# Performance work log

Measured on AMD Instinct MI355X. Metric: run time of the kernel, lower is better.

Reference implementation:

```python
import jax, jax.numpy as jnp
import numpy as np
from jax import lax

VOCAB = 50000; EMB = 256; HID = 256; NLAYERS = 2; OUT = 4
MAXLEN = 32; BATCH = 512; BEAM = 4


def lstm_step(h, c, x, Wih, Whh, bih, bhh):
    # h, c: [L, B, H]; x: [B, E]; torch gate order i, f, g, o
    hs, cs = [], []
    inp = x
    for l in range(Wih.shape[0]):
        g = inp @ Wih[l].T + h[l] @ Whh[l].T + bih[l] + bhh[l]
        i, f, gg, o = jnp.split(g, 4, axis=-1)
        cn = jax.nn.sigmoid(f) * c[l] + jax.nn.sigmoid(i) * jnp.tanh(gg)
        hn = jax.nn.sigmoid(o) * jnp.tanh(cn)
        hs.append(hn); cs.append(cn); inp = hn
    return jnp.stack(hs), jnp.stack(cs), inp


def encode(tokens, emb, Wih, Whh, bih, bhh):
    # tokens: [T, B] int
    x = emb[tokens]  # [T, B, E]
    L, H = Whh.shape[0], Whh.shape[2]
    h0 = jnp.zeros((L, tokens.shape[1], H), x.dtype)

    def step(carry, xt):
        h, c = carry
        h, c, _ = lstm_step(h, c, xt, Wih, Whh, bih, bhh)
        return (h, c), None

    (h, c), _ = lax.scan(step, (h0, h0), x)
    return h, c


def decode_step(tok, h, c, emb, Wih, Whh, bih, bhh, fcW, fcb):
    x = emb[tok]
    h, c, top = lstm_step(h, c, x, Wih, Whh, bih, bhh)
    out = jax.nn.log_softmax(top @ fcW.T + fcb, axis=-1)  # [B', V]
    return out, h, c


def _forward(src, enc_emb, enc_Wih, enc_Whh, enc_bih, enc_bhh,
             dec_emb, dec_Wih, dec_Whh, dec_bih, dec_bhh, dec_fcW, dec_fcb,
             beam_width, teacher_force):
    T, B = src.shape[1], src.shape[2]
    V = dec_fcb.shape[0]
    K = beam_width
    # torch.flip(src[:, 1:, :], [1]): reverse time axis
    h, c = encode(src[0, 1:, :][::-1], enc_emb, enc_Wih, enc_Whh, enc_bih, enc_bhh)

    dec = lambda tok, h, c: decode_step(tok, h, c, dec_emb, dec_Wih, dec_Whh,
                                        dec_bih, dec_bhh, dec_fcW, dec_fcb)

    if teacher_force:
        def step(carry, tok):
            h, c = carry
            out, h, c = dec(tok, h, c)
            return (h, c), out
        _, outs = lax.scan(step, (h, c), src[0])
        return outs

    # --- batch beam search; flat row layout is beam-major: row k*B + b ---
    h = jnp.tile(h, (1, K, 1)); c = jnp.tile(c, (1, K, 1))
    out0, h, c = dec(jnp.tile(src[0, 0, :], K), h, c)  # [B*K, V]
    outputs = jnp.zeros((T, B * K, V), out0.dtype).at[0].set(out0)
    # backtrack[0] = argmax token -> cumulative path score starts at row max
    cum = jnp.max(out0, axis=1)  # [B*K]
    batch_ix = jnp.tile(jnp.arange(B), K)

    def step(carry, xs):
        h, c, cum, outputs = carry
        tok_t, t = xs
        out, h, c = dec(jnp.tile(tok_t, K), h, c)  # [B*K, V]
        probs = cum[:, None] + out  # unnormalized path scores
        # chunk over beams, concat along columns -> [B, K*V]
        probs_b = probs.reshape(K, B, V).transpose(1, 0, 2).reshape(B, K * V)
        lp = (5.0 + t) / 6.0  # length penalty, LP_ALPHA = 1
        _, top_idx = lax.top_k(probs_b / lp, K)  # [B, K]
        rows = (top_idx // V).T.reshape(-1) * B + batch_ix  # [B*K] source rows
        tks = (top_idx % V).T.reshape(-1)  # chosen tokens per new beam row
        h = h[:, rows, :]; c = c[:, rows, :]
        outputs = outputs[:, rows, :].at[t].set(out[rows])
        cum = cum[rows] + out[rows, tks]
        return (h, c, cum, outputs), None

    ts = jnp.arange(1, T)
    (h, c, cum, outputs), _ = lax.scan(step, (h, c, cum, outputs), (src[0, 1:, :], ts))
    return outputs[:, :B, :]


def setup_inputs() -> dict:
    key = jax.random.key(0)
    ks = jax.random.split(key, 16)
    w = lambda k, shape: jax.random.normal(k, shape, jnp.float32) * 0.1
    return {
        'src': jax.random.randint(ks[0], (1, MAXLEN, BATCH), 0, VOCAB),
        'trg': jax.random.randint(ks[1], (MAXLEN, BATCH), 0, OUT),
        'enc_emb': w(ks[2], (VOCAB, EMB)),
        'enc_Wih': w(ks[3], (NLAYERS, 4 * HID, EMB)),
        'enc_Whh': w(ks[4], (NLAYERS, 4 * HID, HID)),
        'enc_bih': w(ks[5], (NLAYERS, 4 * HID)),
        'enc_bhh': w(ks[6], (NLAYERS, 4 * HID)),
        'dec_emb': w(ks[7], (VOCAB, EMB)),
        'dec_Wih': w(ks[8], (NLAYERS, 4 * HID, EMB)),
        'dec_Whh': w(ks[9], (NLAYERS, 4 * HID, HID)),
        'dec_bih': w(ks[10], (NLAYERS, 4 * HID)),
        'dec_bhh': w(ks[11], (NLAYERS, 4 * HID)),
        'dec_fcW': w(ks[12], (OUT, HID)),
        'dec_fcb': w(ks[13], (OUT,)),
        'beam_width': BEAM,
        'teacher_force': 0,
    }


def reference(src, trg, enc_emb, enc_Wih, enc_Whh, enc_bih, enc_bhh,
              dec_emb, dec_Wih, dec_Whh, dec_bih, dec_bhh, dec_fcW, dec_fcb,
              beam_width, teacher_force):
    return _forward(src, enc_emb, enc_Wih, enc_Whh, enc_bih, enc_bhh,
                    dec_emb, dec_Wih, dec_Whh, dec_bih, dec_bhh, dec_fcW, dec_fcb,
                    beam_width, teacher_force)
```

## Files before the change

### kernel.cpp

```cpp
#include <hip/hip_runtime.h>

typedef unsigned short u16;
typedef unsigned int   u32;
typedef __attribute__((ext_vector_type(8))) short bf16x8;
typedef __attribute__((ext_vector_type(4))) float f32x4;

#define DEVINL static __device__ __forceinline__
#define MFMA __builtin_amdgcn_mfma_f32_16x16x32_bf16

DEVINL u16 f2bf(float f){ u32 x = __float_as_uint(f); return (u16)((x + 0x7fffu + ((x>>16)&1u)) >> 16); }
DEVINL float bf2f(u16 u){ return __uint_as_float(((u32)u) << 16); }
DEVINL u32 pack2(float a, float b){ return (u32)f2bf(a) | ((u32)f2bf(b) << 16); }
DEVINL float sigm(float x){ return 1.f/(1.f + __expf(-x)); }
DEVINL float tanhs(float x){ float xc = fminf(fmaxf(x,-15.f),15.f); float e = __expf(2.f*xc); return (e-1.f)/(e+1.f); }
DEVINL void g_store(u32* p, u32 v){ __hip_atomic_store(p, v, __ATOMIC_RELAXED, __HIP_MEMORY_SCOPE_AGENT); }
DEVINL u32  g_load(const u32* p){ return __hip_atomic_load(p, __ATOMIC_RELAXED, __HIP_MEMORY_SCOPE_AGENT); }

__global__ void pack_all(const float* __restrict__ eih, const float* __restrict__ ehh,
                         const float* __restrict__ dih, const float* __restrict__ dhh,
                         const float* __restrict__ ebi, const float* __restrict__ ebh,
                         const float* __restrict__ dbi, const float* __restrict__ dbh,
                         u16* __restrict__ wout, float* __restrict__ bout,
                         u32* __restrict__ flags){
  int blk = blockIdx.x, t = threadIdx.x;
  if (blk < 8192){
    int m = blk >> 10, j2 = blk & 1023;
    const float* base = (m < 4) ? ((m & 1) ? ehh : eih) : ((m & 1) ? dhh : dih);
    const float* S = base + (size_t)((m >> 1) & 1) * 262144;
    int u = j2 >> 2, g = j2 & 3, j = g*256 + u;
    wout[(size_t)blk*256 + t] = f2bf(S[(size_t)j*256 + t]);
  } else if (blk < 8208){
    int idx = (blk - 8192)*256 + t;
    int phase = idx >> 11, l = (idx >> 10) & 1, j2 = idx & 1023;
    int u = j2 >> 2, g = j2 & 3, j = g*256 + u;
    const float* bi = phase ? dbi : ebi;
    const float* bh = phase ? dbh : ebh;
    bout[idx] = bi[l*1024 + j] + bh[l*1024 + j];
  } else {
    for (int i = t; i < 2048; i += 256) flags[i] = 0u;
  }
}

struct SM {
  u16   X[16][264];
  u16   H1t[16][264];
  u16   H2t[16][264];
  float fcw[4][256];
  float fcb[4];
  int   tok[63][16];
};

__global__ void __launch_bounds__(512, 2)
lstm_main(const int* __restrict__ src, const float* __restrict__ enc_emb,
          const float* __restrict__ dec_emb, const u16* __restrict__ wpack,
          const float* __restrict__ bpack, const float* __restrict__ fcW,
          const float* __restrict__ fcb, float* __restrict__ out,
          u32* __restrict__ H1, u32* __restrict__ H2, u32* __restrict__ flags)
{
  __shared__ SM sm;
  const int tid  = threadIdx.x;
  const int wv   = tid >> 6;
  const int lane = tid & 63;
  const int agrp = lane >> 4;
  const int n    = lane & 15;
  const int gid  = blockIdx.x & 31;
  const int w    = blockIdx.x >> 5;
  const int wgb0 = gid << 4;
  const int xr   = tid >> 5, xk = (tid & 31) << 3;
  const int myl  = wv >> 2;
  const int wq   = wv & 3;
  const bool pub = (agrp & 1) == 0;
  const int jrow0 = (w << 7) + (wq << 5) + n;
  const int jrow1 = jrow0 + 16;
  const int uu0   = (w << 5) + (wq << 3) + agrp;
  const int uu1   = uu0 + 4;
  const int pw0   = (w << 4) + (wq << 2) + (agrp >> 1);
  const int pw1   = pw0 + 2;

  for (int i = tid; i < 1008; i += 512){
    int s = i >> 4, b = i & 15;
    int t = (s < 31) ? (31 - s) : (s - 31);
    sm.tok[s][b] = src[t*512 + wgb0 + b];
  }
  for (int i = tid; i < 1024; i += 512) ((float*)sm.fcw)[i] = fcW[i];
  if (tid < 4) sm.fcb[tid] = fcb[tid];
  for (int i = tid; i < 2112; i += 512){
    ((u32*)sm.H1t)[i] = 0u;
    ((u32*)sm.H2t)[i] = 0u;
  }
  __syncthreads();
  {
    int tk = sm.tok[0][xr];
    const float* e = enc_emb + (size_t)tk*256 + xk;
    float4 v0 = *(const float4*)e, v1 = *(const float4*)(e + 4);
    u32* d = (u32*)&sm.X[xr][xk];
    d[0]=pack2(v0.x,v0.y); d[1]=pack2(v0.z,v0.w); d[2]=pack2(v1.x,v1.y); d[3]=pack2(v1.z,v1.w);
  }
  float4 xh0, xh1;
  {
    int tk = sm.tok[1][xr];
    const float* e = enc_emb + (size_t)tk*256 + xk;
    xh0 = *(const float4*)e; xh1 = *(const float4*)(e + 4);
  }

  bf16x8 W[2][16];
  float4 br[2];
  float  cst[2] = {0.f, 0.f};

  auto LOADW = [&](int ph){
    const u16* base = wpack + (size_t)ph*1048576 + (size_t)myl*524288;
    #pragma unroll
    for (int kk = 0; kk < 16; kk++){
      const size_t moff = (size_t)(kk >> 3)*262144 + ((kk & 7) << 5) + (agrp << 3);
      W[0][kk] = *(const bf16x8*)(base + moff + (size_t)jrow0*256);
      W[1][kk] = *(const bf16x8*)(base + moff + (size_t)jrow1*256);
    }
    br[0] = *(const float4*)(bpack + (((ph << 1) + myl) << 10) + (uu0 << 2));
    br[1] = *(const float4*)(bpack + (((ph << 1) + myl) << 10) + (uu1 << 2));
  };
  LOADW(0);
  __syncthreads();

  auto step = [&](int t){
    const bool active = myl ? (t >= 1) : (t <= 62);
    if (active){
      const u16 (*loT)[264] = myl ? sm.H1t : sm.X;
      const u16 (*hiT)[264] = myl ? sm.H2t : sm.H1t;
      f32x4 a0 = {0.f,0.f,0.f,0.f}, a1 = {0.f,0.f,0.f,0.f};
      #pragma unroll
      for (int kk = 0; kk < 8; kk++){
        bf16x8 b = *(const bf16x8*)&loT[n][(kk << 5) + (agrp << 3)];
        a0 = MFMA(W[0][kk], b, a0, 0, 0, 0);
        a1 = MFMA(W[1][kk], b, a1, 0, 0, 0);
      }
      #pragma unroll
      for (int kk = 0; kk < 8; kk++){
        bf16x8 b = *(const bf16x8*)&hiT[n][(kk << 5) + (agrp << 3)];
        a0 = MFMA(W[0][8 + kk], b, a0, 0, 0, 0);
        a1 = MFMA(W[1][8 + kk], b, a1, 0, 0, 0);
      }
      float I0 = sigm(a0[0] + br[0].x), F0 = sigm(a0[1] + br[0].y);
      float G0 = tanhs(a0[2] + br[0].z), O0 = sigm(a0[3] + br[0].w);
      float cn0 = F0*cst[0] + I0*G0; cst[0] = cn0;
      u16 h0 = f2bf(O0 * tanhs(cn0));
      float I1 = sigm(a1[0] + br[1].x), F1 = sigm(a1[1] + br[1].y);
      float G1 = tanhs(a1[2] + br[1].z), O1 = sigm(a1[3] + br[1].w);
      float cn1 = F1*cst[1] + I1*G1; cst[1] = cn1;
      u16 h1b = f2bf(O1 * tanhs(cn1));
      u32 o0 = (u32)__shfl_xor((int)(u32)h0, 16);
      u32 o1 = (u32)__shfl_xor((int)(u32)h1b, 16);
      const int ppar = myl ? ((t + 1) & 1) : (t & 1);
      u32* Hp = (myl ? H2 : H1) + ((size_t)ppar*32 + gid)*2048 + n*128;
      if (pub){
        g_store(Hp + pw0, (u32)h0 | (o0 << 16));
        g_store(Hp + pw1, (u32)h1b | (o1 << 16));
      }
    }
    __syncthreads();
    if (tid == 0) g_store(&flags[gid*8 + w], (u32)(t + 1));
    if (wv == 0){
      const u32 tgt = (u32)(t + 1);
      const bool mine = lane < 8;
      for (;;){
        u32 v = mine ? g_load(&flags[gid*8 + lane]) : tgt;
        if (__all(v >= tgt)) break;
        __builtin_amdgcn_s_sleep(1);
      }
    } else if (wv == 1 && t >= 33){
      const int b = (w << 1) + (lane >> 5), v = (lane >> 3) & 3, q8 = lane & 7;
      const u16* hrow = &sm.H2t[b][q8 << 5];
      const float* wr = &sm.fcw[v][q8 << 5];
      float s = 0.f;
      #pragma unroll
      for (int f = 0; f < 4; f++){
        bf16x8 hv = *(const bf16x8*)(hrow + (f << 3));
        const float4 wa = *(const float4*)(wr + (f << 3));
        const float4 wb = *(const float4*)(wr + (f << 3) + 4);
        s += bf2f((u16)hv[0])*wa.x + bf2f((u16)hv[1])*wa.y
           + bf2f((u16)hv[2])*wa.z + bf2f((u16)hv[3])*wa.w
           + bf2f((u16)hv[4])*wb.x + bf2f((u16)hv[5])*wb.y
           + bf2f((u16)hv[6])*wb.z + bf2f((u16)hv[7])*wb.w;
      }
      s += __shfl_xor(s, 1); s += __shfl_xor(s, 2); s += __shfl_xor(s, 4);
      s += sm.fcb[v];
      float m = fmaxf(s, __shfl_xor(s, 8)); m = fmaxf(m, __shfl_xor(m, 16));
      float e_ = __expf(s - m);
      float es = e_ + __shfl_xor(e_, 8); es += __shfl_xor(es, 16);
      if (q8 == 0)
        out[((size_t)(t - 33)*512 + wgb0 + b)*4 + v] = s - m - __logf(es);
    }
    __syncthreads();
    {
      const int q = tid << 2, r = tid >> 5, p = q & 127;
      if (t < 63){
        const u32* h1r = H1 + ((size_t)(t & 1)*32 + gid)*2048;
        u32 v0 = g_load(h1r+q), v1 = g_load(h1r+q+1), v2 = g_load(h1r+q+2), v3 = g_load(h1r+q+3);
        u32* d1 = (u32*)&sm.H1t[r][p << 1];
        d1[0]=v0; d1[1]=v1; d1[2]=v2; d1[3]=v3;
      }
      if (t > 0){
        const u32* h2r = H2 + ((size_t)((t - 1) & 1)*32 + gid)*2048;
        u32 w0 = g_load(h2r+q), w1 = g_load(h2r+q+1), w2 = g_load(h2r+q+2), w3 = g_load(h2r+q+3);
        u32* d2 = (u32*)&sm.H2t[r][p << 1];
        d2[0]=w0; d2[1]=w1; d2[2]=w2; d2[3]=w3;
      }
      if (t + 1 < 63){
        u32* d = (u32*)&sm.X[xr][xk];
        d[0]=pack2(xh0.x,xh0.y); d[1]=pack2(xh0.z,xh0.w);
        d[2]=pack2(xh1.x,xh1.y); d[3]=pack2(xh1.z,xh1.w);
      }
      if (t + 2 < 63){
        int tk = sm.tok[t+2][xr];
        const float* e = ((t+2) < 31 ? enc_emb : dec_emb) + (size_t)tk*256 + xk;
        xh0 = *(const float4*)e; xh1 = *(const float4*)(e + 4);
      }
    }
    __syncthreads();
  };

  for (int t = 0; t <= 30; ++t) step(t);
  if (myl == 0) LOADW(1);
  step(31);
  if (myl == 1) LOADW(1);
  for (int t = 32; t <= 63; ++t) step(t);

  if (wv == 1){
    const int b = (w << 1) + (lane >> 5), v = (lane >> 3) & 3, q8 = lane & 7;
    const u16* hrow = &sm.H2t[b][q8 << 5];
    const float* wr = &sm.fcw[v][q8 << 5];
    float s = 0.f;
    #pragma unroll
    for (int f = 0; f < 4; f++){
      bf16x8 hv = *(const bf16x8*)(hrow + (f << 3));
      const float4 wa = *(const float4*)(wr + (f << 3));
      const float4 wb = *(const float4*)(wr + (f << 3) + 4);
      s += bf2f((u16)hv[0])*wa.x + bf2f((u16)hv[1])*wa.y
         + bf2f((u16)hv[2])*wa.z + bf2f((u16)hv[3])*wa.w
         + bf2f((u16)hv[4])*wb.x + bf2f((u16)hv[5])*wb.y
         + bf2f((u16)hv[6])*wb.z + bf2f((u16)hv[7])*wb.w;
    }
    s += __shfl_xor(s, 1); s += __shfl_xor(s, 2); s += __shfl_xor(s, 4);
    s += sm.fcb[v];
    float m = fmaxf(s, __shfl_xor(s, 8)); m = fmaxf(m, __shfl_xor(m, 16));
    float e_ = __expf(s - m);
    float es = e_ + __shfl_xor(e_, 8); es += __shfl_xor(es, 16);
    if (q8 == 0)
      out[((size_t)31*512 + wgb0 + b)*4 + v] = s - m - __logf(es);
  }
}

extern "C" void kernel_launch(void* const* d_in, const int* in_sizes, int n_in,
                              void* d_out, int out_size, void* d_ws, size_t ws_size,
                              hipStream_t stream){
  const int*   src     = (const int*)  d_in[0];
  const float* enc_emb = (const float*)d_in[2];
  const float* enc_Wih = (const float*)d_in[3];
  const float* enc_Whh = (const float*)d_in[4];
  const float* enc_bih = (const float*)d_in[5];
  const float* enc_bhh = (const float*)d_in[6];
  const float* dec_emb = (const float*)d_in[7];
  const float* dec_Wih = (const float*)d_in[8];
  const float* dec_Whh = (const float*)d_in[9];
  const float* dec_bih = (const float*)d_in[10];
  const float* dec_bhh = (const float*)d_in[11];
  const float* fcW     = (const float*)d_in[12];
  const float* fcb     = (const float*)d_in[13];
  float* out = (float*)d_out;
  (void)in_sizes; (void)n_in; (void)out_size; (void)ws_size;

  u16*   wpack = (u16*)d_ws;
  float* bpack = (float*)((char*)d_ws + 4194304);
  u32*   H1    = (u32*)((char*)d_ws + 4194304 + 16384);
  u32*   H2    = (u32*)((char*)d_ws + 4194304 + 16384 + 524288);
  u32*   flags = (u32*)((char*)d_ws + 4194304 + 16384 + 1048576);

  pack_all<<<8209, 256, 0, stream>>>(enc_Wih, enc_Whh, dec_Wih, dec_Whh,
                                     enc_bih, enc_bhh, dec_bih, dec_bhh,
                                     wpack, bpack, flags);
  lstm_main<<<256, 512, 0, stream>>>(src, enc_emb, dec_emb, wpack, bpack,
                                     fcW, fcb, out, H1, H2, flags);
}
```

Baseline: 246.6 us.

## Precompute input projection off critical path and split per-layer cross-block sync

Layer-0 waves now compute the input-to-hidden MFMA product for the next timestep after publishing h, so only the recurrent half stays on the critical path. The embedding staging buffer is double-buffered and prefetched one step further ahead to make this possible. Cross-workgroup flag signalling is split into separate flags for layer 1 and layer 2. Each layer's flag is raised by whichever wave finishes last, tracked with a shared-memory atomic counter, and a different wave per layer polls it. The goal is to cut per-step latency of the serial recurrence, at the cost of more LDS, more registers and more complex synchronisation.

```diff
diff --git a/kernel.cpp b/kernel.cpp
--- a/kernel.cpp
+++ b/kernel.cpp
@@ -42,12 +42,13 @@
 }
 
 struct SM {
-  u16   X[16][264];
+  u16   X[2][16][264];
   u16   H1t[16][264];
   u16   H2t[16][264];
   float fcw[4][256];
   float fcb[4];
   int   tok[63][16];
+  u32   C1, C2;
 };
 
 __global__ void __launch_bounds__(512, 2)
@@ -84,24 +85,28 @@
   }
   for (int i = tid; i < 1024; i += 512) ((float*)sm.fcw)[i] = fcW[i];
   if (tid < 4) sm.fcb[tid] = fcb[tid];
+  if (tid == 4){ sm.C1 = 0u; sm.C2 = 0u; }
   for (int i = tid; i < 2112; i += 512){
     ((u32*)sm.H1t)[i] = 0u;
     ((u32*)sm.H2t)[i] = 0u;
   }
   __syncthreads();
   {
-    int tk = sm.tok[0][xr];
+    int tk0 = sm.tok[0][xr];
+    const float* e0 = enc_emb + (size_t)tk0*256 + xk;
+    float4 a0 = *(const float4*)e0, a1 = *(const float4*)(e0 + 4);
+    u32* d0 = (u32*)&sm.X[0][xr][xk];
+    d0[0]=pack2(a0.x,a0.y); d0[1]=pack2(a0.z,a0.w); d0[2]=pack2(a1.x,a1.y); d0[3]=pack2(a1.z,a1.w);
+    int tk1 = sm.tok[1][xr];
+    const float* e1 = enc_emb + (size_t)tk1*256 + xk;
+    float4 b0 = *(const float4*)e1, b1 = *(const float4*)(e1 + 4);
+    u32* d1 = (u32*)&sm.X[1][xr][xk];
+    d1[0]=pack2(b0.x,b0.y); d1[1]=pack2(b0.z,b0.w); d1[2]=pack2(b1.x,b1.y); d1[3]=pack2(b1.z,b1.w);
+  }
+  float4 xh0, xh1;
+  { int tk = sm.tok[2][xr];
     const float* e = enc_emb + (size_t)tk*256 + xk;
-    float4 v0 = *(const float4*)e, v1 = *(const float4*)(e + 4);
-    u32* d = (u32*)&sm.X[xr][xk];
-    d[0]=pack2(v0.x,v0.y); d[1]=pack2(v0.z,v0.w); d[2]=pack2(v1.x,v1.y); d[3]=pack2(v1.z,v1.w);
-  }
-  float4 xh0, xh1;
-  {
-    int tk = sm.tok[1][xr];
-    const float* e = enc_emb + (size_t)tk*256 + xk;
-    xh0 = *(const float4*)e; xh1 = *(const float4*)(e + 4);
-  }
+    xh0 = *(const float4*)e; xh1 = *(const float4*)(e + 4); }
 
   bf16x8 W[2][16];
   float4 br[2];
@@ -121,110 +126,173 @@
   LOADW(0);
   __syncthreads();
 
+  f32x4 gxa = {0.f,0.f,0.f,0.f}, gxb = {0.f,0.f,0.f,0.f};
+  if (myl == 0){
+    #pragma unroll
+    for (int kk = 0; kk < 8; kk++){
+      bf16x8 f = *(const bf16x8*)&sm.X[0][n][(kk << 5) + (agrp << 3)];
+      gxa = MFMA(W[0][kk], f, gxa, 0, 0, 0);
+      gxb = MFMA(W[1][kk], f, gxb, 0, 0, 0);
+    }
+  }
+
   auto step = [&](int t){
-    const bool active = myl ? (t >= 1) : (t <= 62);
-    if (active){
-      const u16 (*loT)[264] = myl ? sm.H1t : sm.X;
-      const u16 (*hiT)[264] = myl ? sm.H2t : sm.H1t;
-      f32x4 a0 = {0.f,0.f,0.f,0.f}, a1 = {0.f,0.f,0.f,0.f};
-      #pragma unroll
-      for (int kk = 0; kk < 8; kk++){
-        bf16x8 b = *(const bf16x8*)&loT[n][(kk << 5) + (agrp << 3)];
-        a0 = MFMA(W[0][kk], b, a0, 0, 0, 0);
-        a1 = MFMA(W[1][kk], b, a1, 0, 0, 0);
-      }
-      #pragma unroll
-      for (int kk = 0; kk < 8; kk++){
-        bf16x8 b = *(const bf16x8*)&hiT[n][(kk << 5) + (agrp << 3)];
-        a0 = MFMA(W[0][8 + kk], b, a0, 0, 0, 0);
-        a1 = MFMA(W[1][8 + kk], b, a1, 0, 0, 0);
-      }
-      float I0 = sigm(a0[0] + br[0].x), F0 = sigm(a0[1] + br[0].y);
-      float G0 = tanhs(a0[2] + br[0].z), O0 = sigm(a0[3] + br[0].w);
-      float cn0 = F0*cst[0] + I0*G0; cst[0] = cn0;
-      u16 h0 = f2bf(O0 * tanhs(cn0));
-      float I1 = sigm(a1[0] + br[1].x), F1 = sigm(a1[1] + br[1].y);
-      float G1 = tanhs(a1[2] + br[1].z), O1 = sigm(a1[3] + br[1].w);
-      float cn1 = F1*cst[1] + I1*G1; cst[1] = cn1;
-      u16 h1b = f2bf(O1 * tanhs(cn1));
-      u32 o0 = (u32)__shfl_xor((int)(u32)h0, 16);
-      u32 o1 = (u32)__shfl_xor((int)(u32)h1b, 16);
-      const int ppar = myl ? ((t + 1) & 1) : (t & 1);
-      u32* Hp = (myl ? H2 : H1) + ((size_t)ppar*32 + gid)*2048 + n*128;
-      if (pub){
-        g_store(Hp + pw0, (u32)h0 | (o0 << 16));
-        g_store(Hp + pw1, (u32)h1b | (o1 << 16));
-      }
-    }
-    __syncthreads();
-    if (tid == 0) g_store(&flags[gid*8 + w], (u32)(t + 1));
-    if (wv == 0){
-      const u32 tgt = (u32)(t + 1);
-      const bool mine = lane < 8;
-      for (;;){
-        u32 v = mine ? g_load(&flags[gid*8 + lane]) : tgt;
-        if (__all(v >= tgt)) break;
-        __builtin_amdgcn_s_sleep(1);
-      }
-    } else if (wv == 1 && t >= 33){
-      const int b = (w << 1) + (lane >> 5), v = (lane >> 3) & 3, q8 = lane & 7;
-      const u16* hrow = &sm.H2t[b][q8 << 5];
-      const float* wr = &sm.fcw[v][q8 << 5];
-      float s = 0.f;
-      #pragma unroll
-      for (int f = 0; f < 4; f++){
-        bf16x8 hv = *(const bf16x8*)(hrow + (f << 3));
-        const float4 wa = *(const float4*)(wr + (f << 3));
-        const float4 wb = *(const float4*)(wr + (f << 3) + 4);
-        s += bf2f((u16)hv[0])*wa.x + bf2f((u16)hv[1])*wa.y
-           + bf2f((u16)hv[2])*wa.z + bf2f((u16)hv[3])*wa.w
-           + bf2f((u16)hv[4])*wb.x + bf2f((u16)hv[5])*wb.y
-           + bf2f((u16)hv[6])*wb.z + bf2f((u16)hv[7])*wb.w;
-      }
-      s += __shfl_xor(s, 1); s += __shfl_xor(s, 2); s += __shfl_xor(s, 4);
-      s += sm.fcb[v];
-      float m = fmaxf(s, __shfl_xor(s, 8)); m = fmaxf(m, __shfl_xor(m, 16));
-      float e_ = __expf(s - m);
-      float es = e_ + __shfl_xor(e_, 8); es += __shfl_xor(es, 16);
-      if (q8 == 0)
-        out[((size_t)(t - 33)*512 + wgb0 + b)*4 + v] = s - m - __logf(es);
+    if (myl == 0){
+      if (t <= 62){
+        bf16x8 hf[8];
+        #pragma unroll
+        for (int kk = 0; kk < 8; kk++)
+          hf[kk] = *(const bf16x8*)&sm.H1t[n][(kk << 5) + (agrp << 3)];
+        f32x4 a0 = gxa, a1 = gxb;
+        #pragma unroll
+        for (int kk = 0; kk < 8; kk++){
+          a0 = MFMA(W[0][8 + kk], hf[kk], a0, 0, 0, 0);
+          a1 = MFMA(W[1][8 + kk], hf[kk], a1, 0, 0, 0);
+        }
+        float I0 = sigm(a0[0] + br[0].x), F0 = sigm(a0[1] + br[0].y);
+        float G0 = tanhs(a0[2] + br[0].z), O0 = sigm(a0[3] + br[0].w);
+        float cn0 = F0*cst[0] + I0*G0; cst[0] = cn0;
+        u16 h0 = f2bf(O0 * tanhs(cn0));
+        float I1 = sigm(a1[0] + br[1].x), F1 = sigm(a1[1] + br[1].y);
+        float G1 = tanhs(a1[2] + br[1].z), O1 = sigm(a1[3] + br[1].w);
+        float cn1 = F1*cst[1] + I1*G1; cst[1] = cn1;
+        u16 h1b = f2bf(O1 * tanhs(cn1));
+        u32 o0 = (u32)__shfl_xor((int)(u32)h0, 16);
+        u32 o1 = (u32)__shfl_xor((int)(u32)h1b, 16);
+        u32* Hp = H1 + ((size_t)(t & 1)*32 + gid)*2048 + n*128;
+        if (pub){
+          g_store(Hp + pw0, (u32)h0 | (o0 << 16));
+          g_store(Hp + pw1, (u32)h1b | (o1 << 16));
+        }
+      }
+      asm volatile("s_waitcnt vmcnt(0)" ::: "memory");
+      if (t <= 62 && lane == 0){
+        u32 old = atomicAdd(&sm.C1, 1u);
+        if (old == (u32)(4*t + 3)) g_store(&flags[gid*8 + w], (u32)(t + 1));
+      }
+      if (t == 30) LOADW(1);
+      if (t <= 61){
+        f32x4 b0 = {0.f,0.f,0.f,0.f}, b1 = {0.f,0.f,0.f,0.f};
+        const int xp = (t + 1) & 1;
+        #pragma unroll
+        for (int kk = 0; kk < 8; kk++){
+          bf16x8 f = *(const bf16x8*)&sm.X[xp][n][(kk << 5) + (agrp << 3)];
+          b0 = MFMA(W[0][kk], f, b0, 0, 0, 0);
+          b1 = MFMA(W[1][kk], f, b1, 0, 0, 0);
+        }
+        gxa = b0; gxb = b1;
+      }
+      if (wv == 0 && t <= 62){
+        const u32 tgt = (u32)(t + 1);
+        const bool mine = lane < 8;
+        for (;;){
+          u32 v = mine ? g_load(&flags[gid*8 + lane]) : tgt;
+          if (__all(v >= tgt)) break;
+          __builtin_amdgcn_s_sleep(1);
+        }
+      }
+    } else {
+      if (t >= 1){
+        f32x4 a0 = {0.f,0.f,0.f,0.f}, a1 = {0.f,0.f,0.f,0.f};
+        #pragma unroll
+        for (int kk = 0; kk < 8; kk++){
+          bf16x8 b = *(const bf16x8*)&sm.H1t[n][(kk << 5) + (agrp << 3)];
+          a0 = MFMA(W[0][kk], b, a0, 0, 0, 0);
+          a1 = MFMA(W[1][kk], b, a1, 0, 0, 0);
+        }
+        #pragma unroll
+        for (int kk = 0; kk < 8; kk++){
+          bf16x8 b = *(const bf16x8*)&sm.H2t[n][(kk << 5) + (agrp << 3)];
+          a0 = MFMA(W[0][8 + kk], b, a0, 0, 0, 0);
+          a1 = MFMA(W[1][8 + kk], b, a1, 0, 0, 0);
+        }
+        float I0 = sigm(a0[0] + br[0].x), F0 = sigm(a0[1] + br[0].y);
+        float G0 = tanhs(a0[2] + br[0].z), O0 = sigm(a0[3] + br[0].w);
+        float cn0 = F0*cst[0] + I0*G0; cst[0] = cn0;
+        u16 h0 = f2bf(O0 * tanhs(cn0));
+        float I1 = sigm(a1[0] + br[1].x), F1 = sigm(a1[1] + br[1].y);
+        float G1 = tanhs(a1[2] + br[1].z), O1 = sigm(a1[3] + br[1].w);
+        float cn1 = F1*cst[1] + I1*G1; cst[1] = cn1;
+        u16 h1b = f2bf(O1 * tanhs(cn1));
+        u32 o0 = (u32)__shfl_xor((int)(u32)h0, 16);
+        u32 o1 = (u32)__shfl_xor((int)(u32)h1b, 16);
+        u32* Hp = H2 + ((size_t)((t + 1) & 1)*32 + gid)*2048 + n*128;
+        if (pub){
+          g_store(Hp + pw0, (u32)h0 | (o0 << 16));
+          g_store(Hp + pw1, (u32)h1b | (o1 << 16));
+        }
+      }
+      asm volatile("s_waitcnt vmcnt(0)" ::: "memory");
+      if (t >= 1 && lane == 0){
+        u32 old = atomicAdd(&sm.C2, 1u);
+        if (old == (u32)(4*t - 1)) g_store(&flags[256 + gid*8 + w], (u32)t);
+      }
+      if (t == 31) LOADW(1);
+      if (wv == 5 && t >= 33){
+        const int b = (w << 1) + (lane >> 5), v = (lane >> 3) & 3, q8 = lane & 7;
+        const u16* hrow = &sm.H2t[b][q8 << 5];
+        const float* wr = &sm.fcw[v][q8 << 5];
+        float s = 0.f;
+        #pragma unroll
+        for (int f = 0; f < 4; f++){
+          bf16x8 hv = *(const bf16x8*)(hrow + (f << 3));
+          const float4 wa = *(const float4*)(wr + (f << 3));
+          const float4 wb = *(const float4*)(wr + (f << 3) + 4);
+          s += bf2f((u16)hv[0])*wa.x + bf2f((u16)hv[1])*wa.y
+             + bf2f((u16)hv[2])*wa.z + bf2f((u16)hv[3])*wa.w
+             + bf2f((u16)hv[4])*wb.x + bf2f((u16)hv[5])*wb.y
+             + bf2f((u16)hv[6])*wb.z + bf2f((u16)hv[7])*wb.w;
+        }
+        s += __shfl_xor(s, 1); s += __shfl_xor(s, 2); s += __shfl_xor(s, 4);
+        s += sm.fcb[v];
+        float m = fmaxf(s, __shfl_xor(s, 8)); m = fmaxf(m, __shfl_xor(m, 16));
+        float e_ = __expf(s - m);
+        float es = e_ + __shfl_xor(e_, 8); es += __shfl_xor(es, 16);
+        if (q8 == 0)
+          out[((size_t)(t - 33)*512 + wgb0 + b)*4 + v] = s - m - __logf(es);
+      }
+      if (wv == 4 && t >= 1){
+        const u32 tgt = (u32)t;
+        const bool mine = lane < 8;
+        for (;;){
+          u32 v = mine ? g_load(&flags[256 + gid*8 + lane]) : tgt;
+          if (__all(v >= tgt)) break;
+          __builtin_amdgcn_s_sleep(1);
+        }
+      }
     }
     __syncthreads();
     {
       const int q = tid << 2, r = tid >> 5, p = q & 127;
-      if (t < 63){
+      if (t <= 62){
         const u32* h1r = H1 + ((size_t)(t & 1)*32 + gid)*2048;
         u32 v0 = g_load(h1r+q), v1 = g_load(h1r+q+1), v2 = g_load(h1r+q+2), v3 = g_load(h1r+q+3);
         u32* d1 = (u32*)&sm.H1t[r][p << 1];
         d1[0]=v0; d1[1]=v1; d1[2]=v2; d1[3]=v3;
       }
-      if (t > 0){
-        const u32* h2r = H2 + ((size_t)((t - 1) & 1)*32 + gid)*2048;
+      if (t >= 1){
+        const u32* h2r = H2 + ((size_t)((t + 1) & 1)*32 + gid)*2048;
         u32 w0 = g_load(h2r+q), w1 = g_load(h2r+q+1), w2 = g_load(h2r+q+2), w3 = g_load(h2r+q+3);
         u32* d2 = (u32*)&sm.H2t[r][p << 1];
         d2[0]=w0; d2[1]=w1; d2[2]=w2; d2[3]=w3;
       }
-      if (t + 1 < 63){
-        u32* d = (u32*)&sm.X[xr][xk];
+      if (t + 2 < 63){
+        u32* d = (u32*)&sm.X[(t + 2) & 1][xr][xk];
         d[0]=pack2(xh0.x,xh0.y); d[1]=pack2(xh0.z,xh0.w);
         d[2]=pack2(xh1.x,xh1.y); d[3]=pack2(xh1.z,xh1.w);
       }
-      if (t + 2 < 63){
-        int tk = sm.tok[t+2][xr];
-        const float* e = ((t+2) < 31 ? enc_emb : dec_emb) + (size_t)tk*256 + xk;
+      if (t + 3 < 63){
+        int tk = sm.tok[t+3][xr];
+        const float* e = ((t+3) < 31 ? enc_emb : dec_emb) + (size_t)tk*256 + xk;
         xh0 = *(const float4*)e; xh1 = *(const float4*)(e + 4);
       }
     }
     __syncthreads();
   };
 
-  for (int t = 0; t <= 30; ++t) step(t);
-  if (myl == 0) LOADW(1);
-  step(31);
-  if (myl == 1) LOADW(1);
-  for (int t = 32; t <= 63; ++t) step(t);
-
-  if (wv == 1){
+  for (int t = 0; t <= 63; ++t) step(t);
+
+  if (wv == 5){
     const int b = (w << 1) + (lane >> 5), v = (lane >> 3) & 3, q8 = lane & 7;
     const u16* hrow = &sm.H2t[b][q8 << 5];
     const float* wr = &sm.fcw[v][q8 << 5];
```

Result: slower. 384.7 us (+56.0%).

## Replace flag barrier with step-stamped hidden-state words and double-buffered LDS

Applied to the files above, without the earlier changes.

Drops the per-step flag publish/poll barrier and one block-wide syncthreads. Each hidden-state word now carries a 32-bit step stamp in a 64-bit atomic store, so consumers spin directly on the data until every stamp matches. Shared-memory X/H1/H2 tiles are double-buffered by step parity, which lets the next step's inputs be written while the current ones are still being read. This doubles global hidden-state traffic and LDS usage. Every thread now polls its own data rather than one wave polling flags.

```diff
diff --git a/kernel.cpp b/kernel.cpp
--- a/kernel.cpp
+++ b/kernel.cpp
@@ -2,6 +2,7 @@
 
 typedef unsigned short u16;
 typedef unsigned int   u32;
+typedef unsigned long long u64;
 typedef __attribute__((ext_vector_type(8))) short bf16x8;
 typedef __attribute__((ext_vector_type(4))) float f32x4;
 
@@ -13,15 +14,15 @@
 DEVINL u32 pack2(float a, float b){ return (u32)f2bf(a) | ((u32)f2bf(b) << 16); }
 DEVINL float sigm(float x){ return 1.f/(1.f + __expf(-x)); }
 DEVINL float tanhs(float x){ float xc = fminf(fmaxf(x,-15.f),15.f); float e = __expf(2.f*xc); return (e-1.f)/(e+1.f); }
-DEVINL void g_store(u32* p, u32 v){ __hip_atomic_store(p, v, __ATOMIC_RELAXED, __HIP_MEMORY_SCOPE_AGENT); }
-DEVINL u32  g_load(const u32* p){ return __hip_atomic_load(p, __ATOMIC_RELAXED, __HIP_MEMORY_SCOPE_AGENT); }
+DEVINL void g_store64(u64* p, u64 v){ __hip_atomic_store(p, v, __ATOMIC_RELAXED, __HIP_MEMORY_SCOPE_AGENT); }
+DEVINL u64  g_load64(const u64* p){ return __hip_atomic_load(p, __ATOMIC_RELAXED, __HIP_MEMORY_SCOPE_AGENT); }
 
 __global__ void pack_all(const float* __restrict__ eih, const float* __restrict__ ehh,
                          const float* __restrict__ dih, const float* __restrict__ dhh,
                          const float* __restrict__ ebi, const float* __restrict__ ebh,
                          const float* __restrict__ dbi, const float* __restrict__ dbh,
                          u16* __restrict__ wout, float* __restrict__ bout,
-                         u32* __restrict__ flags){
+                         u32* __restrict__ Hz){
   int blk = blockIdx.x, t = threadIdx.x;
   if (blk < 8192){
     int m = blk >> 10, j2 = blk & 1023;
@@ -37,14 +38,15 @@
     const float* bh = phase ? dbh : ebh;
     bout[idx] = bi[l*1024 + j] + bh[l*1024 + j];
   } else {
-    for (int i = t; i < 2048; i += 256) flags[i] = 0u;
+    int idx = (blk - 8208)*256 + t;
+    Hz[idx] = 0u;
   }
 }
 
 struct SM {
-  u16   X[16][264];
-  u16   H1t[16][264];
-  u16   H2t[16][264];
+  u16   X[2][16][264];
+  u16   H1t[2][16][264];
+  u16   H2t[2][16][264];
   float fcw[4][256];
   float fcb[4];
   int   tok[63][16];
@@ -55,7 +57,7 @@
           const float* __restrict__ dec_emb, const u16* __restrict__ wpack,
           const float* __restrict__ bpack, const float* __restrict__ fcW,
           const float* __restrict__ fcb, float* __restrict__ out,
-          u32* __restrict__ H1, u32* __restrict__ H2, u32* __restrict__ flags)
+          u64* __restrict__ H1c, u64* __restrict__ H2c)
 {
   __shared__ SM sm;
   const int tid  = threadIdx.x;
@@ -85,15 +87,15 @@
   for (int i = tid; i < 1024; i += 512) ((float*)sm.fcw)[i] = fcW[i];
   if (tid < 4) sm.fcb[tid] = fcb[tid];
   for (int i = tid; i < 2112; i += 512){
-    ((u32*)sm.H1t)[i] = 0u;
-    ((u32*)sm.H2t)[i] = 0u;
+    ((u32*)sm.H1t[0])[i] = 0u;
+    ((u32*)sm.H2t[0])[i] = 0u;
   }
   __syncthreads();
   {
     int tk = sm.tok[0][xr];
     const float* e = enc_emb + (size_t)tk*256 + xk;
     float4 v0 = *(const float4*)e, v1 = *(const float4*)(e + 4);
-    u32* d = (u32*)&sm.X[xr][xk];
+    u32* d = (u32*)&sm.X[0][xr][xk];
     d[0]=pack2(v0.x,v0.y); d[1]=pack2(v0.z,v0.w); d[2]=pack2(v1.x,v1.y); d[3]=pack2(v1.z,v1.w);
   }
   float4 xh0, xh1;
@@ -122,10 +124,11 @@
   __syncthreads();
 
   auto step = [&](int t){
+    const int par = t & 1, parW = par ^ 1;
     const bool active = myl ? (t >= 1) : (t <= 62);
     if (active){
-      const u16 (*loT)[264] = myl ? sm.H1t : sm.X;
-      const u16 (*hiT)[264] = myl ? sm.H2t : sm.H1t;
+      const u16 (*loT)[264] = myl ? sm.H1t[par] : sm.X[par];
+      const u16 (*hiT)[264] = myl ? sm.H2t[par] : sm.H1t[par];
       f32x4 a0 = {0.f,0.f,0.f,0.f}, a1 = {0.f,0.f,0.f,0.f};
       #pragma unroll
       for (int kk = 0; kk < 8; kk++){
@@ -149,26 +152,17 @@
       u16 h1b = f2bf(O1 * tanhs(cn1));
       u32 o0 = (u32)__shfl_xor((int)(u32)h0, 16);
       u32 o1 = (u32)__shfl_xor((int)(u32)h1b, 16);
-      const int ppar = myl ? ((t + 1) & 1) : (t & 1);
-      u32* Hp = (myl ? H2 : H1) + ((size_t)ppar*32 + gid)*2048 + n*128;
+      const int ppar = myl ? ((t + 1) & 1) : par;
+      u64* Hp = (myl ? H2c : H1c) + (((size_t)ppar*32 + gid)*16 + n)*128;
       if (pub){
-        g_store(Hp + pw0, (u32)h0 | (o0 << 16));
-        g_store(Hp + pw1, (u32)h1b | (o1 << 16));
-      }
-    }
-    __syncthreads();
-    if (tid == 0) g_store(&flags[gid*8 + w], (u32)(t + 1));
-    if (wv == 0){
-      const u32 tgt = (u32)(t + 1);
-      const bool mine = lane < 8;
-      for (;;){
-        u32 v = mine ? g_load(&flags[gid*8 + lane]) : tgt;
-        if (__all(v >= tgt)) break;
-        __builtin_amdgcn_s_sleep(1);
-      }
-    } else if (wv == 1 && t >= 33){
+        const u64 stamp = (u64)(u32)(t + 1) << 32;
+        g_store64(Hp + pw0, (u64)((u32)h0  | (o0 << 16)) | stamp);
+        g_store64(Hp + pw1, (u64)((u32)h1b | (o1 << 16)) | stamp);
+      }
+    }
+    if (wv == 1 && t >= 33){
       const int b = (w << 1) + (lane >> 5), v = (lane >> 3) & 3, q8 = lane & 7;
-      const u16* hrow = &sm.H2t[b][q8 << 5];
+      const u16* hrow = &sm.H2t[par][b][q8 << 5];
       const float* wr = &sm.fcw[v][q8 << 5];
       float s = 0.f;
       #pragma unroll
@@ -189,31 +183,44 @@
       if (q8 == 0)
         out[((size_t)(t - 33)*512 + wgb0 + b)*4 + v] = s - m - __logf(es);
     }
-    __syncthreads();
-    {
-      const int q = tid << 2, r = tid >> 5, p = q & 127;
-      if (t < 63){
-        const u32* h1r = H1 + ((size_t)(t & 1)*32 + gid)*2048;
-        u32 v0 = g_load(h1r+q), v1 = g_load(h1r+q+1), v2 = g_load(h1r+q+2), v3 = g_load(h1r+q+3);
-        u32* d1 = (u32*)&sm.H1t[r][p << 1];
-        d1[0]=v0; d1[1]=v1; d1[2]=v2; d1[3]=v3;
-      }
-      if (t > 0){
-        const u32* h2r = H2 + ((size_t)((t - 1) & 1)*32 + gid)*2048;
-        u32 w0 = g_load(h2r+q), w1 = g_load(h2r+q+1), w2 = g_load(h2r+q+2), w3 = g_load(h2r+q+3);
-        u32* d2 = (u32*)&sm.H2t[r][p << 1];
-        d2[0]=w0; d2[1]=w1; d2[2]=w2; d2[3]=w3;
-      }
-      if (t + 1 < 63){
-        u32* d = (u32*)&sm.X[xr][xk];
-        d[0]=pack2(xh0.x,xh0.y); d[1]=pack2(xh0.z,xh0.w);
-        d[2]=pack2(xh1.x,xh1.y); d[3]=pack2(xh1.z,xh1.w);
-      }
-      if (t + 2 < 63){
-        int tk = sm.tok[t+2][xr];
-        const float* e = ((t+2) < 31 ? enc_emb : dec_emb) + (size_t)tk*256 + xk;
-        xh0 = *(const float4*)e; xh1 = *(const float4*)(e + 4);
-      }
+    const int q = tid << 2;
+    const int r = tid >> 5, p = q & 127;
+    const u32 st = (u32)(t + 1);
+    if (t < 63){
+      const u64* h1r = H1c + ((size_t)par*32 + gid)*2048 + q;
+      u64 a0, a1, a2, a3;
+      for (;;){
+        a0 = g_load64(h1r+0); a1 = g_load64(h1r+1);
+        a2 = g_load64(h1r+2); a3 = g_load64(h1r+3);
+        if ((u32)(a0>>32)==st && (u32)(a1>>32)==st &&
+            (u32)(a2>>32)==st && (u32)(a3>>32)==st) break;
+        __builtin_amdgcn_s_sleep(1);
+      }
+      u32* d1 = (u32*)&sm.H1t[parW][r][p << 1];
+      d1[0]=(u32)a0; d1[1]=(u32)a1; d1[2]=(u32)a2; d1[3]=(u32)a3;
+    }
+    if (t >= 1){
+      const u64* h2r = H2c + ((size_t)((t - 1) & 1)*32 + gid)*2048 + q;
+      u64 b0, b1, b2, b3;
+      for (;;){
+        b0 = g_load64(h2r+0); b1 = g_load64(h2r+1);
+        b2 = g_load64(h2r+2); b3 = g_load64(h2r+3);
+        if ((u32)(b0>>32)==st && (u32)(b1>>32)==st &&
+            (u32)(b2>>32)==st && (u32)(b3>>32)==st) break;
+        __builtin_amdgcn_s_sleep(1);
+      }
+      u32* d2 = (u32*)&sm.H2t[parW][r][p << 1];
+      d2[0]=(u32)b0; d2[1]=(u32)b1; d2[2]=(u32)b2; d2[3]=(u32)b3;
+    }
+    if (t + 1 < 63){
+      u32* d = (u32*)&sm.X[parW][xr][xk];
+      d[0]=pack2(xh0.x,xh0.y); d[1]=pack2(xh0.z,xh0.w);
+      d[2]=pack2(xh1.x,xh1.y); d[3]=pack2(xh1.z,xh1.w);
+    }
+    if (t + 2 < 63){
+      int tk = sm.tok[t+2][xr];
+      const float* e = ((t+2) < 31 ? enc_emb : dec_emb) + (size_t)tk*256 + xk;
+      xh0 = *(const float4*)e; xh1 = *(const float4*)(e + 4);
     }
     __syncthreads();
   };
@@ -226,7 +233,7 @@
 
   if (wv == 1){
     const int b = (w << 1) + (lane >> 5), v = (lane >> 3) & 3, q8 = lane & 7;
-    const u16* hrow = &sm.H2t[b][q8 << 5];
+    const u16* hrow = &sm.H2t[0][b][q8 << 5];
     const float* wr = &sm.fcw[v][q8 << 5];
     float s = 0.f;
     #pragma unroll
@@ -270,13 +277,13 @@
 
   u16*   wpack = (u16*)d_ws;
   float* bpack = (float*)((char*)d_ws + 4194304);
-  u32*   H1    = (u32*)((char*)d_ws + 4194304 + 16384);
-  u32*   H2    = (u32*)((char*)d_ws + 4194304 + 16384 + 524288);
-  u32*   flags = (u32*)((char*)d_ws + 4194304 + 16384 + 1048576);
-
-  pack_all<<<8209, 256, 0, stream>>>(enc_Wih, enc_Whh, dec_Wih, dec_Whh,
-                                     enc_bih, enc_bhh, dec_bih, dec_bhh,
-                                     wpack, bpack, flags);
+  u64*   H1c   = (u64*)((char*)d_ws + 4194304 + 16384);
+  u64*   H2c   = H1c + 131072;
+  u32*   Hz    = (u32*)H1c;
+
+  pack_all<<<10256, 256, 0, stream>>>(enc_Wih, enc_Whh, dec_Wih, dec_Whh,
+                                      enc_bih, enc_bhh, dec_bih, dec_bhh,
+                                      wpack, bpack, Hz);
   lstm_main<<<256, 512, 0, stream>>>(src, enc_emb, dec_emb, wpack, bpack,
-                                     fcW, fcb, out, H1, H2, flags);
+                                     fcW, fcb, out, H1c, H2c);
 }
```

Result: slower. 663.8 us (+169.2%).
